# Kernel optimization log

Hardware: AMD Instinct MI355X
Metric: run time of the kernel (lower is better)

The kernel has to match this reference:

```python
import jax, jax.numpy as jnp
import numpy as np


def setup_inputs() -> dict:
    key = jax.random.key(0)
    k1, k2 = jax.random.split(key)
    N, D, E = 16384, 4096, 64  # tokens, n_embd, n_exp
    x = jax.random.normal(k1, (N, D), dtype=jnp.float32)
    W = jax.random.normal(k2, (E, D), dtype=jnp.float32) * 0.02  # w_gate weight [n_exp, n_embd]
    return {"x": x, "W": W, "top_k": 4, "n_groups": 8, "n_limited_groups": 4}


def reference(x, W, top_k, n_groups, n_limited_groups):
    ROUTE_SCALE = 1.0
    N = x.shape[0]
    E = W.shape[0]
    exp_per_group = E // n_groups

    logits = x @ W.T                      # [N, E] gate linear (bias=False)
    scores = jax.nn.softmax(logits, -1)   # func == 'softmax'

    # group-limited routing: pick top n_limited_groups groups by max score (bias=False path)
    gs = scores.reshape(N, n_groups, exp_per_group)
    group_scores = gs.max(axis=-1)                             # [N, G]
    _, top_grp = jax.lax.top_k(group_scores, n_limited_groups)  # [N, L]
    selected = jnp.any(
        jnp.arange(n_groups)[None, None, :] == top_grp[:, :, None], axis=1
    )                                                           # [N, G] bool
    masked = jnp.where(selected[:, :, None], gs, -jnp.inf).reshape(N, E)

    # top-k experts over unmasked scores; weights are the gathered scores
    topk_vals, topk_idx = jax.lax.top_k(masked, top_k)          # [N, K]
    weights = (topk_vals * ROUTE_SCALE).astype(x.dtype)         # softmax -> no renorm

    # histc over expert ids
    counts = jnp.zeros((E,), jnp.int32).at[topk_idx.reshape(-1)].add(1)
    return weights, topk_idx, counts
```

## Files before the change

### kernel.cpp

```cpp
#include <hip/hip_runtime.h>
#include <math.h>

#define NTOK 16384
#define DDIM 4096
#define NEXP 64
#define KTOP 4

#define SPLITK 8
#define KPER (DDIM / SPLITK)
#define BK 32
#define NSTG (KPER / BK)
#define BMB 256

typedef __attribute__((ext_vector_type(8))) short short8;
typedef __attribute__((ext_vector_type(4))) float f32x4;


__device__ __forceinline__ unsigned short f2bf_rtn(float x) {
    unsigned int b = __float_as_uint(x);
    return (unsigned short)((b + 0x7FFFu + ((b >> 16) & 1u)) >> 16);
}
__device__ __forceinline__ float bf2f(unsigned short h) {
    return __uint_as_float(((unsigned int)h) << 16);
}
__device__ __forceinline__ short8 mk8(unsigned int a, unsigned int b,
                                      unsigned int c, unsigned int d) {
    union { unsigned int u[4]; short8 s; } p;
    p.u[0] = a; p.u[1] = b; p.u[2] = c; p.u[3] = d;
    return p.s;
}
__device__ __forceinline__ void gl2lds16(const void* g, void* l) {
    __builtin_amdgcn_global_load_lds(
        (const __attribute__((address_space(1))) unsigned int*)g,
        (__attribute__((address_space(3))) unsigned int*)l, 16, 0, 0);
}

__global__ __launch_bounds__(256) void prep_kernel(
    const float* __restrict__ W, unsigned short* __restrict__ Whi,
    unsigned short* __restrict__ Wlo, float* __restrict__ counts)
{
    int idx = blockIdx.x * 256 + threadIdx.x;
    float x = W[idx];
    unsigned short h = f2bf_rtn(x);
    float lo = x - bf2f(h);
    Whi[idx] = h;
    Wlo[idx] = f2bf_rtn(lo);
    if (blockIdx.x == 0 && threadIdx.x < NEXP) counts[threadIdx.x] = 0.0f;
}

__global__ __launch_bounds__(512, 4) void gemm_kernel(
    const float* __restrict__ X, const unsigned short* __restrict__ Whi,
    const unsigned short* __restrict__ Wlo, float* __restrict__ part)
{
    __shared__ float          sX[2][BMB * BK];
    __shared__ unsigned short sH[2][NEXP * BK];
    __shared__ unsigned short sL[2][NEXP * BK];

    const int tid  = threadIdx.x;
    const int lane = tid & 63;
    const int w    = tid >> 6;
    const int tb   = blockIdx.x >> 3;
    const int s    = blockIdx.x & 7;
    const int kbase = s * KPER;
    const int tok0 = tb * BMB;

    const float* xsrc[4];
    int xdst[4];
    #pragma unroll
    for (int i = 0; i < 4; ++i) {
        const int seg = i * 8 + w;
        const int o   = seg * 256 + lane * 4;
        const int row = o >> 5;
        const int cp  = o & 31;
        const int sw  = ((row & 4) << 1) | ((row & 8) >> 1);
        xsrc[i] = X + (size_t)(tok0 + row) * DDIM + kbase + (cp ^ sw);
        xdst[i] = seg * 256;
    }
    const int wseg = w & 3;
    const int wo   = wseg * 512 + lane * 8;
    const int we   = wo >> 5;
    const int wkk  = wo & 31;
    const unsigned short* wsrc =
        ((w < 4) ? Whi : Wlo) + (size_t)we * DDIM + kbase + (wkk ^ ((we & 3) * 8));

    #pragma unroll
    for (int i = 0; i < 4; ++i) gl2lds16(xsrc[i], &sX[0][xdst[i]]);
    gl2lds16(wsrc, (w < 4) ? (void*)&sH[0][wseg * 512] : (void*)&sL[0][wseg * 512]);
    __syncthreads();

    const int fr = lane & 15;
    const int fg = lane >> 4;
    const int sw  = ((fr & 4) << 1) | ((fr & 8) >> 1);
    const int fo0 = (fg * 8) ^ sw;
    const int fo1 = (fg * 8 + 4) ^ sw;
    const int frow0 = (w * 32 + fr) * BK;
    const int frow1 = frow0 + 16 * BK;
    const int bt  = (fg * 8) ^ ((fr & 3) * 8);

    f32x4 acc[2][4];
    #pragma unroll
    for (int mg = 0; mg < 2; ++mg)
        #pragma unroll
        for (int ng = 0; ng < 4; ++ng)
            acc[mg][ng] = (f32x4){0.f, 0.f, 0.f, 0.f};

    for (int st = 0; st < NSTG; ++st) {
        const float*          cx = sX[st & 1];
        const unsigned short* ch = sH[st & 1];
        const unsigned short* cl = sL[st & 1];

        if (st + 1 < NSTG) {
            const int nb = (st + 1) & 1;
            #pragma unroll
            for (int i = 0; i < 4; ++i)
                gl2lds16(xsrc[i] + (st + 1) * BK, &sX[nb][xdst[i]]);
            gl2lds16(wsrc + (st + 1) * BK,
                     (w < 4) ? (void*)&sH[nb][wseg * 512]
                             : (void*)&sL[nb][wseg * 512]);
        }

        const float4 a00 = *(const float4*)&cx[frow0 + fo0];
        const float4 a01 = *(const float4*)&cx[frow0 + fo1];
        const float4 a10 = *(const float4*)&cx[frow1 + fo0];
        const float4 a11 = *(const float4*)&cx[frow1 + fo1];

        short8 ahi[2], alo[2];
        #pragma unroll
        for (int mg = 0; mg < 2; ++mg) {
            const float4 qa = mg ? a10 : a00;
            const float4 qb = mg ? a11 : a01;
            unsigned int hi[4], lo[4];
            const unsigned int u0 = __float_as_uint(qa.x), u1 = __float_as_uint(qa.y);
            const unsigned int u2 = __float_as_uint(qa.z), u3 = __float_as_uint(qa.w);
            const unsigned int u4 = __float_as_uint(qb.x), u5 = __float_as_uint(qb.y);
            const unsigned int u6 = __float_as_uint(qb.z), u7 = __float_as_uint(qb.w);
            hi[0] = (u0 >> 16) | (u1 & 0xFFFF0000u);
            hi[1] = (u2 >> 16) | (u3 & 0xFFFF0000u);
            hi[2] = (u4 >> 16) | (u5 & 0xFFFF0000u);
            hi[3] = (u6 >> 16) | (u7 & 0xFFFF0000u);
            const float l0 = qa.x - __uint_as_float(u0 & 0xFFFF0000u);
            const float l1 = qa.y - __uint_as_float(u1 & 0xFFFF0000u);
            const float l2 = qa.z - __uint_as_float(u2 & 0xFFFF0000u);
            const float l3 = qa.w - __uint_as_float(u3 & 0xFFFF0000u);
            const float l4 = qb.x - __uint_as_float(u4 & 0xFFFF0000u);
            const float l5 = qb.y - __uint_as_float(u5 & 0xFFFF0000u);
            const float l6 = qb.z - __uint_as_float(u6 & 0xFFFF0000u);
            const float l7 = qb.w - __uint_as_float(u7 & 0xFFFF0000u);
            lo[0] = (__float_as_uint(l0) >> 16) | (__float_as_uint(l1) & 0xFFFF0000u);
            lo[1] = (__float_as_uint(l2) >> 16) | (__float_as_uint(l3) & 0xFFFF0000u);
            lo[2] = (__float_as_uint(l4) >> 16) | (__float_as_uint(l5) & 0xFFFF0000u);
            lo[3] = (__float_as_uint(l6) >> 16) | (__float_as_uint(l7) & 0xFFFF0000u);
            ahi[mg] = mk8(hi[0], hi[1], hi[2], hi[3]);
            alo[mg] = mk8(lo[0], lo[1], lo[2], lo[3]);
        }

        #pragma unroll
        for (int ng = 0; ng < 4; ++ng) {
            const int bo = (ng * 16 + fr) * BK + bt;
            const short8 bh = *(const short8*)&ch[bo];
            const short8 bl = *(const short8*)&cl[bo];
            #pragma unroll
            for (int mg = 0; mg < 2; ++mg) {
                acc[mg][ng] = __builtin_amdgcn_mfma_f32_16x16x32_bf16(
                    ahi[mg], bh, acc[mg][ng], 0, 0, 0);
                acc[mg][ng] = __builtin_amdgcn_mfma_f32_16x16x32_bf16(
                    ahi[mg], bl, acc[mg][ng], 0, 0, 0);
                acc[mg][ng] = __builtin_amdgcn_mfma_f32_16x16x32_bf16(
                    alo[mg], bh, acc[mg][ng], 0, 0, 0);
            }
        }

        __syncthreads();
    }

    #pragma unroll
    for (int mg = 0; mg < 2; ++mg)
        #pragma unroll
        for (int r = 0; r < 4; ++r) {
            const int row = tok0 + w * 32 + mg * 16 + fg * 4 + r;
            float* __restrict__ pp = part + ((size_t)row * SPLITK + s) * NEXP;
            #pragma unroll
            for (int ng = 0; ng < 4; ++ng)
                pp[ng * 16 + fr] = acc[mg][ng][r];
        }
}

__global__ __launch_bounds__(256) void route_kernel(
    const float* __restrict__ part, float* __restrict__ outW,
    float* __restrict__ outI, float* __restrict__ counts)
{
    __shared__ int hist[NEXP];
    const int tid = threadIdx.x;
    if (tid < NEXP) hist[tid] = 0;
    __syncthreads();

    const int lane = tid & 63;
    const int wv   = tid >> 6;
    const int tok_base = blockIdx.x * 32 + wv * 8;

    for (int t = 0; t < 8; ++t) {
        const int n = tok_base + t;
        float L = 0.0f;
        #pragma unroll
        for (int s = 0; s < SPLITK; ++s)
            L += part[((size_t)n * SPLITK + s) * NEXP + lane];

        float m = L;
        #pragma unroll
        for (int off = 32; off > 0; off >>= 1) m = fmaxf(m, __shfl_xor(m, off));
        float p = expf(L - m);
        float ssum = p;
        #pragma unroll
        for (int off = 32; off > 0; off >>= 1) ssum += __shfl_xor(ssum, off);
        float score = p / ssum;

        float gm = score;
        gm = fmaxf(gm, __shfl_xor(gm, 1));
        gm = fmaxf(gm, __shfl_xor(gm, 2));
        gm = fmaxf(gm, __shfl_xor(gm, 4));

        float ga[8];
        #pragma unroll
        for (int g = 0; g < 8; ++g) ga[g] = __shfl(gm, g * 8);
        unsigned selmask = 0u;
        #pragma unroll
        for (int r = 0; r < 4; ++r) {
            float best = -INFINITY; int bg = 0;
            #pragma unroll
            for (int g = 0; g < 8; ++g) {
                bool taken  = (selmask >> g) & 1u;
                bool better = (!taken) && (ga[g] > best);
                bg   = better ? g : bg;
                best = better ? ga[g] : best;
            }
            selmask |= (1u << bg);
        }

        float ms = ((selmask >> (lane >> 3)) & 1u) ? score : -INFINITY;
        float wk[4]; int wi[4];
        #pragma unroll
        for (int r = 0; r < 4; ++r) {
            float v = ms; int ix = lane;
            #pragma unroll
            for (int off = 32; off > 0; off >>= 1) {
                float vo = __shfl_xor(v, off);
                int   io = __shfl_xor(ix, off);
                if (vo > v || (vo == v && io < ix)) { v = vo; ix = io; }
            }
            wk[r] = v; wi[r] = ix;
            if (lane == ix) ms = -INFINITY;
        }

        if (lane == 0) {
            *(float4*)&outW[(size_t)n * 4] = make_float4(wk[0], wk[1], wk[2], wk[3]);
            *(float4*)&outI[(size_t)n * 4] =
                make_float4((float)wi[0], (float)wi[1], (float)wi[2], (float)wi[3]);
            atomicAdd(&hist[wi[0]], 1);
            atomicAdd(&hist[wi[1]], 1);
            atomicAdd(&hist[wi[2]], 1);
            atomicAdd(&hist[wi[3]], 1);
        }
    }

    __syncthreads();
    if (tid < NEXP) atomicAdd(&counts[tid], (float)hist[tid]);
}

extern "C" void kernel_launch(void* const* d_in, const int* in_sizes, int n_in,
                              void* d_out, int out_size, void* d_ws, size_t ws_size,
                              hipStream_t stream) {
    const float* X = (const float*)d_in[0];
    const float* W = (const float*)d_in[1];

    float* outW   = (float*)d_out;
    float* outI   = outW + (size_t)NTOK * KTOP;
    float* counts = outW + (size_t)2 * NTOK * KTOP;

    float*          part = (float*)d_ws;
    unsigned short* Whi  = (unsigned short*)(part + (size_t)NTOK * SPLITK * NEXP);
    unsigned short* Wlo  = Whi + (size_t)NEXP * DDIM;

    prep_kernel<<<(NEXP * DDIM) / 256, 256, 0, stream>>>(W, Whi, Wlo, counts);
    gemm_kernel<<<(NTOK / BMB) * SPLITK, 512, 0, stream>>>(X, Whi, Wlo, part);
    route_kernel<<<NTOK / 32, 256, 0, stream>>>(part, outW, outI, counts);
}
```

Before: 101.3 us.

## Fuse gate GEMM and routing into one kernel without split-K partials

Replaces the split-K GEMM plus separate route kernel with a single kernel. Each 512-thread block computes full-K logits for 64 tokens over all 64 experts with BK=128, keeps them in LDS, then runs softmax, group top-k and the histogram in place. This removes the 32 MB partial-logit write/read round trip and one launch. The cost is fewer blocks (256), lower occupancy (launch bounds 2), and each block streaming both weight halves along the full K dimension.

```diff
diff --git a/kernel.cpp b/kernel.cpp
--- a/kernel.cpp
+++ b/kernel.cpp
@@ -6,11 +6,10 @@
 #define NEXP 64
 #define KTOP 4
 
-#define SPLITK 8
-#define KPER (DDIM / SPLITK)
-#define BK 32
-#define NSTG (KPER / BK)
-#define BMB 256
+#define BK   128
+#define NSTG (DDIM / BK)
+#define TPB  64
+#define NBLK (NTOK / TPB)
 
 typedef __attribute__((ext_vector_type(8))) short short8;
 typedef __attribute__((ext_vector_type(4))) float f32x4;
@@ -48,61 +47,67 @@
     if (blockIdx.x == 0 && threadIdx.x < NEXP) counts[threadIdx.x] = 0.0f;
 }
 
-__global__ __launch_bounds__(512, 4) void gemm_kernel(
+__global__ __launch_bounds__(512, 2) void gate_kernel(
     const float* __restrict__ X, const unsigned short* __restrict__ Whi,
-    const unsigned short* __restrict__ Wlo, float* __restrict__ part)
+    const unsigned short* __restrict__ Wlo, float* __restrict__ outW,
+    float* __restrict__ outI, float* __restrict__ counts)
 {
-    __shared__ float          sX[2][BMB * BK];
+    __shared__ float          sX[2][TPB * BK];
     __shared__ unsigned short sH[2][NEXP * BK];
     __shared__ unsigned short sL[2][NEXP * BK];
+    __shared__ float          lgt[TPB][66];
+    __shared__ int            hist[NEXP];
 
     const int tid  = threadIdx.x;
     const int lane = tid & 63;
     const int w    = tid >> 6;
-    const int tb   = blockIdx.x >> 3;
-    const int s    = blockIdx.x & 7;
-    const int kbase = s * KPER;
-    const int tok0 = tb * BMB;
+    const int wm   = w >> 2;
+    const int wn   = w & 3;
+    const int tok0 = blockIdx.x * TPB;
+
+    if (tid < NEXP) hist[tid] = 0;
 
     const float* xsrc[4];
-    int xdst[4];
+    int xdstf[4];
     #pragma unroll
     for (int i = 0; i < 4; ++i) {
-        const int seg = i * 8 + w;
-        const int o   = seg * 256 + lane * 4;
-        const int row = o >> 5;
-        const int cp  = o & 31;
-        const int sw  = ((row & 4) << 1) | ((row & 8) >> 1);
-        xsrc[i] = X + (size_t)(tok0 + row) * DDIM + kbase + (cp ^ sw);
-        xdst[i] = seg * 256;
-    }
-    const int wseg = w & 3;
-    const int wo   = wseg * 512 + lane * 8;
-    const int we   = wo >> 5;
-    const int wkk  = wo & 31;
-    const unsigned short* wsrc =
-        ((w < 4) ? Whi : Wlo) + (size_t)we * DDIM + kbase + (wkk ^ ((we & 3) * 8));
-
-    #pragma unroll
-    for (int i = 0; i < 4; ++i) gl2lds16(xsrc[i], &sX[0][xdst[i]]);
-    gl2lds16(wsrc, (w < 4) ? (void*)&sH[0][wseg * 512] : (void*)&sL[0][wseg * 512]);
+        const int seg = w * 4 + i;
+        const int r0  = seg * 2 + (lane >> 5);
+        const int pc  = lane & 31;
+        xsrc[i]  = X + (size_t)(tok0 + r0) * DDIM + ((pc ^ (r0 & 15)) * 4);
+        xdstf[i] = seg * 256;
+    }
+    const unsigned short *whsrc[2], *wlsrc[2];
+    int wdsts[2];
+    #pragma unroll
+    for (int j = 0; j < 2; ++j) {
+        const int seg2 = w * 2 + j;
+        const int e    = seg2 * 4 + (lane >> 4);
+        const int sc   = lane & 15;
+        const size_t o = (size_t)e * DDIM + ((sc ^ (e & 15)) * 8);
+        whsrc[j] = Whi + o;
+        wlsrc[j] = Wlo + o;
+        wdsts[j] = seg2 * 512;
+    }
+
+    #pragma unroll
+    for (int i = 0; i < 4; ++i) gl2lds16(xsrc[i], &sX[0][xdstf[i]]);
+    #pragma unroll
+    for (int j = 0; j < 2; ++j) {
+        gl2lds16(whsrc[j], &sH[0][wdsts[j]]);
+        gl2lds16(wlsrc[j], &sL[0][wdsts[j]]);
+    }
     __syncthreads();
 
     const int fr = lane & 15;
     const int fg = lane >> 4;
-    const int sw  = ((fr & 4) << 1) | ((fr & 8) >> 1);
-    const int fo0 = (fg * 8) ^ sw;
-    const int fo1 = (fg * 8 + 4) ^ sw;
-    const int frow0 = (w * 32 + fr) * BK;
-    const int frow1 = frow0 + 16 * BK;
-    const int bt  = (fg * 8) ^ ((fr & 3) * 8);
-
-    f32x4 acc[2][4];
-    #pragma unroll
-    for (int mg = 0; mg < 2; ++mg)
-        #pragma unroll
-        for (int ng = 0; ng < 4; ++ng)
-            acc[mg][ng] = (f32x4){0.f, 0.f, 0.f, 0.f};
+    const int rowA0 = (wm * 32 + fr) * BK;
+    const int rowA1 = rowA0 + 16 * BK;
+    const int eB    = (wn * 16 + fr) * BK;
+
+    f32x4 acc[2];
+    acc[0] = (f32x4){0.f, 0.f, 0.f, 0.f};
+    acc[1] = (f32x4){0.f, 0.f, 0.f, 0.f};
 
     for (int st = 0; st < NSTG; ++st) {
         const float*          cx = sX[st & 1];
@@ -111,62 +116,63 @@
 
         if (st + 1 < NSTG) {
             const int nb = (st + 1) & 1;
+            const int ko = (st + 1) * BK;
             #pragma unroll
             for (int i = 0; i < 4; ++i)
-                gl2lds16(xsrc[i] + (st + 1) * BK, &sX[nb][xdst[i]]);
-            gl2lds16(wsrc + (st + 1) * BK,
-                     (w < 4) ? (void*)&sH[nb][wseg * 512]
-                             : (void*)&sL[nb][wseg * 512]);
-        }
-
-        const float4 a00 = *(const float4*)&cx[frow0 + fo0];
-        const float4 a01 = *(const float4*)&cx[frow0 + fo1];
-        const float4 a10 = *(const float4*)&cx[frow1 + fo0];
-        const float4 a11 = *(const float4*)&cx[frow1 + fo1];
-
-        short8 ahi[2], alo[2];
-        #pragma unroll
-        for (int mg = 0; mg < 2; ++mg) {
-            const float4 qa = mg ? a10 : a00;
-            const float4 qb = mg ? a11 : a01;
-            unsigned int hi[4], lo[4];
-            const unsigned int u0 = __float_as_uint(qa.x), u1 = __float_as_uint(qa.y);
-            const unsigned int u2 = __float_as_uint(qa.z), u3 = __float_as_uint(qa.w);
-            const unsigned int u4 = __float_as_uint(qb.x), u5 = __float_as_uint(qb.y);
-            const unsigned int u6 = __float_as_uint(qb.z), u7 = __float_as_uint(qb.w);
-            hi[0] = (u0 >> 16) | (u1 & 0xFFFF0000u);
-            hi[1] = (u2 >> 16) | (u3 & 0xFFFF0000u);
-            hi[2] = (u4 >> 16) | (u5 & 0xFFFF0000u);
-            hi[3] = (u6 >> 16) | (u7 & 0xFFFF0000u);
-            const float l0 = qa.x - __uint_as_float(u0 & 0xFFFF0000u);
-            const float l1 = qa.y - __uint_as_float(u1 & 0xFFFF0000u);
-            const float l2 = qa.z - __uint_as_float(u2 & 0xFFFF0000u);
-            const float l3 = qa.w - __uint_as_float(u3 & 0xFFFF0000u);
-            const float l4 = qb.x - __uint_as_float(u4 & 0xFFFF0000u);
-            const float l5 = qb.y - __uint_as_float(u5 & 0xFFFF0000u);
-            const float l6 = qb.z - __uint_as_float(u6 & 0xFFFF0000u);
-            const float l7 = qb.w - __uint_as_float(u7 & 0xFFFF0000u);
-            lo[0] = (__float_as_uint(l0) >> 16) | (__float_as_uint(l1) & 0xFFFF0000u);
-            lo[1] = (__float_as_uint(l2) >> 16) | (__float_as_uint(l3) & 0xFFFF0000u);
-            lo[2] = (__float_as_uint(l4) >> 16) | (__float_as_uint(l5) & 0xFFFF0000u);
-            lo[3] = (__float_as_uint(l6) >> 16) | (__float_as_uint(l7) & 0xFFFF0000u);
-            ahi[mg] = mk8(hi[0], hi[1], hi[2], hi[3]);
-            alo[mg] = mk8(lo[0], lo[1], lo[2], lo[3]);
-        }
-
-        #pragma unroll
-        for (int ng = 0; ng < 4; ++ng) {
-            const int bo = (ng * 16 + fr) * BK + bt;
-            const short8 bh = *(const short8*)&ch[bo];
-            const short8 bl = *(const short8*)&cl[bo];
+                gl2lds16(xsrc[i] + ko, &sX[nb][xdstf[i]]);
+            #pragma unroll
+            for (int j = 0; j < 2; ++j) {
+                gl2lds16(whsrc[j] + ko, &sH[nb][wdsts[j]]);
+                gl2lds16(wlsrc[j] + ko, &sL[nb][wdsts[j]]);
+            }
+        }
+
+        #pragma unroll
+        for (int ks = 0; ks < 4; ++ks) {
+            const int ch0 = ks * 8 + fg * 2;
+            const float4 a00 = *(const float4*)&cx[rowA0 + ((ch0     ) ^ fr) * 4];
+            const float4 a01 = *(const float4*)&cx[rowA0 + ((ch0 + 1) ^ fr) * 4];
+            const float4 a10 = *(const float4*)&cx[rowA1 + ((ch0     ) ^ fr) * 4];
+            const float4 a11 = *(const float4*)&cx[rowA1 + ((ch0 + 1) ^ fr) * 4];
+
+            short8 ahi[2], alo[2];
             #pragma unroll
             for (int mg = 0; mg < 2; ++mg) {
-                acc[mg][ng] = __builtin_amdgcn_mfma_f32_16x16x32_bf16(
-                    ahi[mg], bh, acc[mg][ng], 0, 0, 0);
-                acc[mg][ng] = __builtin_amdgcn_mfma_f32_16x16x32_bf16(
-                    ahi[mg], bl, acc[mg][ng], 0, 0, 0);
-                acc[mg][ng] = __builtin_amdgcn_mfma_f32_16x16x32_bf16(
-                    alo[mg], bh, acc[mg][ng], 0, 0, 0);
+                const float4 qa = mg ? a10 : a00;
+                const float4 qb = mg ? a11 : a01;
+                const unsigned int u0 = __float_as_uint(qa.x), u1 = __float_as_uint(qa.y);
+                const unsigned int u2 = __float_as_uint(qa.z), u3 = __float_as_uint(qa.w);
+                const unsigned int u4 = __float_as_uint(qb.x), u5 = __float_as_uint(qb.y);
+                const unsigned int u6 = __float_as_uint(qb.z), u7 = __float_as_uint(qb.w);
+                unsigned int hi0 = (u0 >> 16) | (u1 & 0xFFFF0000u);
+                unsigned int hi1 = (u2 >> 16) | (u3 & 0xFFFF0000u);
+                unsigned int hi2 = (u4 >> 16) | (u5 & 0xFFFF0000u);
+                unsigned int hi3 = (u6 >> 16) | (u7 & 0xFFFF0000u);
+                const float l0 = qa.x - __uint_as_float(u0 & 0xFFFF0000u);
+                const float l1 = qa.y - __uint_as_float(u1 & 0xFFFF0000u);
+                const float l2 = qa.z - __uint_as_float(u2 & 0xFFFF0000u);
+                const float l3 = qa.w - __uint_as_float(u3 & 0xFFFF0000u);
+                const float l4 = qb.x - __uint_as_float(u4 & 0xFFFF0000u);
+                const float l5 = qb.y - __uint_as_float(u5 & 0xFFFF0000u);
+                const float l6 = qb.z - __uint_as_float(u6 & 0xFFFF0000u);
+                const float l7 = qb.w - __uint_as_float(u7 & 0xFFFF0000u);
+                unsigned int lo0 = (__float_as_uint(l0) >> 16) | (__float_as_uint(l1) & 0xFFFF0000u);
+                unsigned int lo1 = (__float_as_uint(l2) >> 16) | (__float_as_uint(l3) & 0xFFFF0000u);
+                unsigned int lo2 = (__float_as_uint(l4) >> 16) | (__float_as_uint(l5) & 0xFFFF0000u);
+                unsigned int lo3 = (__float_as_uint(l6) >> 16) | (__float_as_uint(l7) & 0xFFFF0000u);
+                ahi[mg] = mk8(hi0, hi1, hi2, hi3);
+                alo[mg] = mk8(lo0, lo1, lo2, lo3);
+            }
+
+            const int cb = (ks * 4 + fg) ^ fr;
+            const short8 bh = *(const short8*)&ch[eB + cb * 8];
+            const short8 bl = *(const short8*)&cl[eB + cb * 8];
+
+            #pragma unroll
+            for (int mg = 0; mg < 2; ++mg) {
+                acc[mg] = __builtin_amdgcn_mfma_f32_16x16x32_bf16(ahi[mg], bh, acc[mg], 0, 0, 0);
+                acc[mg] = __builtin_amdgcn_mfma_f32_16x16x32_bf16(ahi[mg], bl, acc[mg], 0, 0, 0);
+                acc[mg] = __builtin_amdgcn_mfma_f32_16x16x32_bf16(alo[mg], bh, acc[mg], 0, 0, 0);
             }
         }
 
@@ -176,34 +182,14 @@
     #pragma unroll
     for (int mg = 0; mg < 2; ++mg)
         #pragma unroll
-        for (int r = 0; r < 4; ++r) {
-            const int row = tok0 + w * 32 + mg * 16 + fg * 4 + r;
-            float* __restrict__ pp = part + ((size_t)row * SPLITK + s) * NEXP;
-            #pragma unroll
-            for (int ng = 0; ng < 4; ++ng)
-                pp[ng * 16 + fr] = acc[mg][ng][r];
-        }
-}
-
-__global__ __launch_bounds__(256) void route_kernel(
-    const float* __restrict__ part, float* __restrict__ outW,
-    float* __restrict__ outI, float* __restrict__ counts)
-{
-    __shared__ int hist[NEXP];
-    const int tid = threadIdx.x;
-    if (tid < NEXP) hist[tid] = 0;
+        for (int r = 0; r < 4; ++r)
+            lgt[wm * 32 + mg * 16 + fg * 4 + r][wn * 16 + fr] = acc[mg][r];
     __syncthreads();
 
-    const int lane = tid & 63;
-    const int wv   = tid >> 6;
-    const int tok_base = blockIdx.x * 32 + wv * 8;
-
     for (int t = 0; t < 8; ++t) {
-        const int n = tok_base + t;
-        float L = 0.0f;
-        #pragma unroll
-        for (int s = 0; s < SPLITK; ++s)
-            L += part[((size_t)n * SPLITK + s) * NEXP + lane];
+        const int nl = w * 8 + t;
+        const int n  = tok0 + nl;
+        const float L = lgt[nl][lane];
 
         float m = L;
         #pragma unroll
@@ -212,7 +198,7 @@
         float ssum = p;
         #pragma unroll
         for (int off = 32; off > 0; off >>= 1) ssum += __shfl_xor(ssum, off);
-        float score = p / ssum;
+        const float score = p / ssum;
 
         float gm = score;
         gm = fmaxf(gm, __shfl_xor(gm, 1));
@@ -276,11 +262,9 @@
     float* outI   = outW + (size_t)NTOK * KTOP;
     float* counts = outW + (size_t)2 * NTOK * KTOP;
 
-    float*          part = (float*)d_ws;
-    unsigned short* Whi  = (unsigned short*)(part + (size_t)NTOK * SPLITK * NEXP);
-    unsigned short* Wlo  = Whi + (size_t)NEXP * DDIM;
+    unsigned short* Whi = (unsigned short*)d_ws;
+    unsigned short* Wlo = Whi + (size_t)NEXP * DDIM;
 
     prep_kernel<<<(NEXP * DDIM) / 256, 256, 0, stream>>>(W, Whi, Wlo, counts);
-    gemm_kernel<<<(NTOK / BMB) * SPLITK, 512, 0, stream>>>(X, Whi, Wlo, part);
-    route_kernel<<<NTOK / 32, 256, 0, stream>>>(part, outW, outI, counts);
-}
+    gate_kernel<<<NBLK, 512, 0, stream>>>(X, Whi, Wlo, outW, outI, counts);
+}
```

Result: slower. 120.3 us (+18.8%).

## Keep the W K-slice resident in LDS and pipeline X per wave

Applied to the files above, without the earlier changes.

The GEMM now loads each block's whole bf16 hi/lo W K-slice into LDS once. X tiles stream through per-wave private double buffers, ordered by explicit vmcnt and lgkmcnt waits, so the main loop needs no block-wide barriers. Split-K goes from 8 to 16 and blocks shrink to 4 waves of 16 rows each. This removes __syncthreads stalls and repeated W staging. In exchange the partial-logit buffer doubles in size, which the route kernel must write and read back, and larger LDS use per block lowers resident waves.

```diff
diff --git a/kernel.cpp b/kernel.cpp
--- a/kernel.cpp
+++ b/kernel.cpp
@@ -6,11 +6,14 @@
 #define NEXP 64
 #define KTOP 4
 
-#define SPLITK 8
+#define SPLITK 16
 #define KPER (DDIM / SPLITK)
 #define BK 32
 #define NSTG (KPER / BK)
-#define BMB 256
+#define WROWS 16
+#define NWAVE 4
+#define TPB (WROWS * NWAVE)
+#define NBLK ((NTOK / TPB) * SPLITK)
 
 typedef __attribute__((ext_vector_type(8))) short short8;
 typedef __attribute__((ext_vector_type(4))) float f32x4;
@@ -48,141 +51,124 @@
     if (blockIdx.x == 0 && threadIdx.x < NEXP) counts[threadIdx.x] = 0.0f;
 }
 
-__global__ __launch_bounds__(512, 4) void gemm_kernel(
+__global__ __launch_bounds__(256, 2) void gemm_kernel(
     const float* __restrict__ X, const unsigned short* __restrict__ Whi,
     const unsigned short* __restrict__ Wlo, float* __restrict__ part)
 {
-    __shared__ float          sX[2][BMB * BK];
-    __shared__ unsigned short sH[2][NEXP * BK];
-    __shared__ unsigned short sL[2][NEXP * BK];
+    __shared__ unsigned short sH[NEXP * KPER];
+    __shared__ unsigned short sL[NEXP * KPER];
+    __shared__ float sXa[NWAVE][2][WROWS * BK];
 
     const int tid  = threadIdx.x;
     const int lane = tid & 63;
     const int w    = tid >> 6;
-    const int tb   = blockIdx.x >> 3;
-    const int s    = blockIdx.x & 7;
+    const int tb   = blockIdx.x >> 4;
+    const int s    = blockIdx.x & 15;
     const int kbase = s * KPER;
-    const int tok0 = tb * BMB;
-
-    const float* xsrc[4];
-    int xdst[4];
-    #pragma unroll
-    for (int i = 0; i < 4; ++i) {
-        const int seg = i * 8 + w;
-        const int o   = seg * 256 + lane * 4;
-        const int row = o >> 5;
-        const int cp  = o & 31;
-        const int sw  = ((row & 4) << 1) | ((row & 8) >> 1);
-        xsrc[i] = X + (size_t)(tok0 + row) * DDIM + kbase + (cp ^ sw);
-        xdst[i] = seg * 256;
-    }
-    const int wseg = w & 3;
-    const int wo   = wseg * 512 + lane * 8;
-    const int we   = wo >> 5;
-    const int wkk  = wo & 31;
-    const unsigned short* wsrc =
-        ((w < 4) ? Whi : Wlo) + (size_t)we * DDIM + kbase + (wkk ^ ((we & 3) * 8));
-
-    #pragma unroll
-    for (int i = 0; i < 4; ++i) gl2lds16(xsrc[i], &sX[0][xdst[i]]);
-    gl2lds16(wsrc, (w < 4) ? (void*)&sH[0][wseg * 512] : (void*)&sL[0][wseg * 512]);
+    const int wtok  = tb * TPB + w * WROWS;
+
+    #pragma unroll
+    for (int i = 0; i < 8; ++i) {
+        const int g  = i * 256 + tid;
+        const int e  = g >> 5;
+        const int p  = g & 31;
+        const int gb = (i * 256 + (tid >> 6) * 64) * 8;
+        const size_t src = (size_t)e * DDIM + kbase + ((p ^ (e & 7)) << 3);
+        gl2lds16(Whi + src, &sH[gb]);
+        gl2lds16(Wlo + src, &sL[gb]);
+    }
+
+    const int xrow = (lane >> 3);
+    const int xp   = lane & 7;
+    const float* xsrc0 = X + (size_t)(wtok + xrow) * DDIM + kbase
+                       + ((xp ^ (xrow & 7)) << 2);
+    const float* xsrc1 = X + (size_t)(wtok + 8 + xrow) * DDIM + kbase
+                       + ((xp ^ ((xrow + 8) & 7)) << 2);
+    float* const xb0 = &sXa[w][0][0];
+    float* const xb1 = &sXa[w][1][0];
+
+#define ISSUE_X(buf, st)                                                    \
+    {                                                                       \
+        gl2lds16(xsrc0 + (st) * BK, (buf));                                 \
+        gl2lds16(xsrc1 + (st) * BK, (buf) + 256);                           \
+    }
+
+    ISSUE_X(xb0, 0)
+    ISSUE_X(xb1, 1)
     __syncthreads();
 
     const int fr = lane & 15;
     const int fg = lane >> 4;
-    const int sw  = ((fr & 4) << 1) | ((fr & 8) >> 1);
-    const int fo0 = (fg * 8) ^ sw;
-    const int fo1 = (fg * 8 + 4) ^ sw;
-    const int frow0 = (w * 32 + fr) * BK;
-    const int frow1 = frow0 + 16 * BK;
-    const int bt  = (fg * 8) ^ ((fr & 3) * 8);
-
-    f32x4 acc[2][4];
-    #pragma unroll
-    for (int mg = 0; mg < 2; ++mg)
+    const int xkey = fr & 7;
+
+    f32x4 acc[4];
+    #pragma unroll
+    for (int ng = 0; ng < 4; ++ng) acc[ng] = (f32x4){0.f, 0.f, 0.f, 0.f};
+
+    #pragma unroll
+    for (int st = 0; st < NSTG; ++st) {
+        if (st < NSTG - 1) {
+            asm volatile("s_waitcnt vmcnt(2)" ::: "memory");
+        } else {
+            asm volatile("s_waitcnt vmcnt(0)" ::: "memory");
+        }
+        __builtin_amdgcn_sched_barrier(0);
+
+        const float* cx = (st & 1) ? xb1 : xb0;
+
+        const float4 qa = *(const float4*)&cx[fr * BK + (((fg * 2    ) ^ xkey) << 2)];
+        const float4 qb = *(const float4*)&cx[fr * BK + (((fg * 2 + 1) ^ xkey) << 2)];
+
+        const unsigned int u0 = __float_as_uint(qa.x), u1 = __float_as_uint(qa.y);
+        const unsigned int u2 = __float_as_uint(qa.z), u3 = __float_as_uint(qa.w);
+        const unsigned int u4 = __float_as_uint(qb.x), u5 = __float_as_uint(qb.y);
+        const unsigned int u6 = __float_as_uint(qb.z), u7 = __float_as_uint(qb.w);
+        const short8 ahi = mk8((u0 >> 16) | (u1 & 0xFFFF0000u),
+                               (u2 >> 16) | (u3 & 0xFFFF0000u),
+                               (u4 >> 16) | (u5 & 0xFFFF0000u),
+                               (u6 >> 16) | (u7 & 0xFFFF0000u));
+        const float l0 = qa.x - __uint_as_float(u0 & 0xFFFF0000u);
+        const float l1 = qa.y - __uint_as_float(u1 & 0xFFFF0000u);
+        const float l2 = qa.z - __uint_as_float(u2 & 0xFFFF0000u);
+        const float l3 = qa.w - __uint_as_float(u3 & 0xFFFF0000u);
+        const float l4 = qb.x - __uint_as_float(u4 & 0xFFFF0000u);
+        const float l5 = qb.y - __uint_as_float(u5 & 0xFFFF0000u);
+        const float l6 = qb.z - __uint_as_float(u6 & 0xFFFF0000u);
+        const float l7 = qb.w - __uint_as_float(u7 & 0xFFFF0000u);
+        const short8 alo = mk8(
+            (__float_as_uint(l0) >> 16) | (__float_as_uint(l1) & 0xFFFF0000u),
+            (__float_as_uint(l2) >> 16) | (__float_as_uint(l3) & 0xFFFF0000u),
+            (__float_as_uint(l4) >> 16) | (__float_as_uint(l5) & 0xFFFF0000u),
+            (__float_as_uint(l6) >> 16) | (__float_as_uint(l7) & 0xFFFF0000u));
+
+        #pragma unroll
+        for (int ng = 0; ng < 4; ++ng) {
+            const int e  = ng * 16 + fr;
+            const int so = e * KPER + (((st * 4 + fg) ^ xkey) << 3);
+            const short8 bh = *(const short8*)&sH[so];
+            const short8 bl = *(const short8*)&sL[so];
+            acc[ng] = __builtin_amdgcn_mfma_f32_16x16x32_bf16(ahi, bh, acc[ng], 0, 0, 0);
+            acc[ng] = __builtin_amdgcn_mfma_f32_16x16x32_bf16(ahi, bl, acc[ng], 0, 0, 0);
+            acc[ng] = __builtin_amdgcn_mfma_f32_16x16x32_bf16(alo, bh, acc[ng], 0, 0, 0);
+        }
+
+        if (st + 2 < NSTG) {
+            asm volatile("s_waitcnt lgkmcnt(0)" ::: "memory");
+            __builtin_amdgcn_sched_barrier(0);
+            float* nb = (st & 1) ? xb1 : xb0;
+            ISSUE_X(nb, st + 2)
+        }
+    }
+#undef ISSUE_X
+
+    #pragma unroll
+    for (int r = 0; r < 4; ++r) {
+        const int n = wtok + fg * 4 + r;
+        float* __restrict__ pp = part + ((size_t)n * SPLITK + s) * NEXP;
         #pragma unroll
         for (int ng = 0; ng < 4; ++ng)
-            acc[mg][ng] = (f32x4){0.f, 0.f, 0.f, 0.f};
-
-    for (int st = 0; st < NSTG; ++st) {
-        const float*          cx = sX[st & 1];
-        const unsigned short* ch = sH[st & 1];
-        const unsigned short* cl = sL[st & 1];
-
-        if (st + 1 < NSTG) {
-            const int nb = (st + 1) & 1;
-            #pragma unroll
-            for (int i = 0; i < 4; ++i)
-                gl2lds16(xsrc[i] + (st + 1) * BK, &sX[nb][xdst[i]]);
-            gl2lds16(wsrc + (st + 1) * BK,
-                     (w < 4) ? (void*)&sH[nb][wseg * 512]
-                             : (void*)&sL[nb][wseg * 512]);
-        }
-
-        const float4 a00 = *(const float4*)&cx[frow0 + fo0];
-        const float4 a01 = *(const float4*)&cx[frow0 + fo1];
-        const float4 a10 = *(const float4*)&cx[frow1 + fo0];
-        const float4 a11 = *(const float4*)&cx[frow1 + fo1];
-
-        short8 ahi[2], alo[2];
-        #pragma unroll
-        for (int mg = 0; mg < 2; ++mg) {
-            const float4 qa = mg ? a10 : a00;
-            const float4 qb = mg ? a11 : a01;
-            unsigned int hi[4], lo[4];
-            const unsigned int u0 = __float_as_uint(qa.x), u1 = __float_as_uint(qa.y);
-            const unsigned int u2 = __float_as_uint(qa.z), u3 = __float_as_uint(qa.w);
-            const unsigned int u4 = __float_as_uint(qb.x), u5 = __float_as_uint(qb.y);
-            const unsigned int u6 = __float_as_uint(qb.z), u7 = __float_as_uint(qb.w);
-            hi[0] = (u0 >> 16) | (u1 & 0xFFFF0000u);
-            hi[1] = (u2 >> 16) | (u3 & 0xFFFF0000u);
-            hi[2] = (u4 >> 16) | (u5 & 0xFFFF0000u);
-            hi[3] = (u6 >> 16) | (u7 & 0xFFFF0000u);
-            const float l0 = qa.x - __uint_as_float(u0 & 0xFFFF0000u);
-            const float l1 = qa.y - __uint_as_float(u1 & 0xFFFF0000u);
-            const float l2 = qa.z - __uint_as_float(u2 & 0xFFFF0000u);
-            const float l3 = qa.w - __uint_as_float(u3 & 0xFFFF0000u);
-            const float l4 = qb.x - __uint_as_float(u4 & 0xFFFF0000u);
-            const float l5 = qb.y - __uint_as_float(u5 & 0xFFFF0000u);
-            const float l6 = qb.z - __uint_as_float(u6 & 0xFFFF0000u);
-            const float l7 = qb.w - __uint_as_float(u7 & 0xFFFF0000u);
-            lo[0] = (__float_as_uint(l0) >> 16) | (__float_as_uint(l1) & 0xFFFF0000u);
-            lo[1] = (__float_as_uint(l2) >> 16) | (__float_as_uint(l3) & 0xFFFF0000u);
-            lo[2] = (__float_as_uint(l4) >> 16) | (__float_as_uint(l5) & 0xFFFF0000u);
-            lo[3] = (__float_as_uint(l6) >> 16) | (__float_as_uint(l7) & 0xFFFF0000u);
-            ahi[mg] = mk8(hi[0], hi[1], hi[2], hi[3]);
-            alo[mg] = mk8(lo[0], lo[1], lo[2], lo[3]);
-        }
-
-        #pragma unroll
-        for (int ng = 0; ng < 4; ++ng) {
-            const int bo = (ng * 16 + fr) * BK + bt;
-            const short8 bh = *(const short8*)&ch[bo];
-            const short8 bl = *(const short8*)&cl[bo];
-            #pragma unroll
-            for (int mg = 0; mg < 2; ++mg) {
-                acc[mg][ng] = __builtin_amdgcn_mfma_f32_16x16x32_bf16(
-                    ahi[mg], bh, acc[mg][ng], 0, 0, 0);
-                acc[mg][ng] = __builtin_amdgcn_mfma_f32_16x16x32_bf16(
-                    ahi[mg], bl, acc[mg][ng], 0, 0, 0);
-                acc[mg][ng] = __builtin_amdgcn_mfma_f32_16x16x32_bf16(
-                    alo[mg], bh, acc[mg][ng], 0, 0, 0);
-            }
-        }
-
-        __syncthreads();
-    }
-
-    #pragma unroll
-    for (int mg = 0; mg < 2; ++mg)
-        #pragma unroll
-        for (int r = 0; r < 4; ++r) {
-            const int row = tok0 + w * 32 + mg * 16 + fg * 4 + r;
-            float* __restrict__ pp = part + ((size_t)row * SPLITK + s) * NEXP;
-            #pragma unroll
-            for (int ng = 0; ng < 4; ++ng)
-                pp[ng * 16 + fr] = acc[mg][ng][r];
-        }
+            pp[ng * 16 + fr] = acc[ng][r];
+    }
 }
 
 __global__ __launch_bounds__(256) void route_kernel(
@@ -212,7 +198,7 @@
         float ssum = p;
         #pragma unroll
         for (int off = 32; off > 0; off >>= 1) ssum += __shfl_xor(ssum, off);
-        float score = p / ssum;
+        const float score = p / ssum;
 
         float gm = score;
         gm = fmaxf(gm, __shfl_xor(gm, 1));
@@ -281,6 +267,6 @@
     unsigned short* Wlo  = Whi + (size_t)NEXP * DDIM;
 
     prep_kernel<<<(NEXP * DDIM) / 256, 256, 0, stream>>>(W, Whi, Wlo, counts);
-    gemm_kernel<<<(NTOK / BMB) * SPLITK, 512, 0, stream>>>(X, Whi, Wlo, part);
+    gemm_kernel<<<NBLK, 256, 0, stream>>>(X, Whi, Wlo, part);
     route_kernel<<<NTOK / 32, 256, 0, stream>>>(part, outW, outI, counts);
 }
```

After: 115.1 us. 1.14x slower.
